# Optimization experiments

Hardware: AMD Instinct MI355X
Metric: run time of the kernel (lower is better)

## Reference

```python
import jax, jax.numpy as jnp
import numpy as np

EPS_NORM = 1e-4
EPS_LOG = 1e-6


def normed_weight(W):
    # W: [O, I, K] (K=1). normalize() over dims (1,2) per output channel,
    # with norm scaled by alpha = sqrt(O / (O*I*K)) = 1/sqrt(I*K), then
    # divided again by sqrt(I*K) in get_normed_weight (eval path).
    O, I, K = W.shape
    fan_in = I * K
    norm = jnp.sqrt(jnp.sum(jnp.square(W), axis=(1, 2), keepdims=True))  # [O,1,1]
    norm = EPS_NORM + norm / np.sqrt(fan_in)
    return (W / norm) / np.sqrt(fan_in)


def complex_log(x):
    real = jnp.log(jnp.maximum(jnp.abs(x), EPS_LOG))
    imag = jnp.where(x < 0, jnp.pi, 0.0).astype(real.dtype)
    return jax.lax.complex(real, imag)


def logcumsumexp_complex(z, axis=-1):
    # stable complex logcumsumexp via associative scan:
    # logaddexp(a, b) = m + log(exp(a-m) + exp(b-m)), m = max(Re a, Re b)
    def combine(a, b):
        m = jnp.maximum(a.real, b.real)
        mc = jax.lax.complex(m, jnp.zeros_like(m))
        return mc + jnp.log(jnp.exp(a - mc) + jnp.exp(b - mc))
    return jax.lax.associative_scan(combine, z, axis=axis)


def min_gru(h, g):
    # h, g: [B, C, L]; parallel log-space minGRU recurrence along L
    log_scale = 0.5 * jnp.log(1.0 / jnp.cosh(g) + 1.0)
    log_coeffs = -jax.nn.softplus(g) + log_scale                 # real
    log_values = (-jax.nn.softplus(-g) + log_scale) + complex_log(h)  # complex
    a_star = jnp.cumsum(log_coeffs, axis=-1)                     # real
    a_star_c = jax.lax.complex(a_star, jnp.zeros_like(a_star))
    log_h = a_star_c + logcumsumexp_complex(log_values - a_star_c, axis=-1)
    return jnp.exp(log_h).real


def scaled_cat(xs, axis):
    Ns = [x.shape[axis] for x in xs]
    scale = np.sqrt(np.mean(Ns))
    return scale * jnp.concatenate([x * n ** -0.5 for n, x in zip(Ns, xs)], axis=axis)


def setup_inputs() -> dict:
    key = jax.random.key(0)
    k1, k2 = jax.random.split(key)
    B, D, L = 8, 512, 8192
    x = jax.random.normal(k1, (B, D, L), dtype=jnp.float32)
    W = jax.random.normal(k2, (2 * D, D, 1), dtype=jnp.float32)  # Conv1d(dim, 2*dim, 1) weight
    return {"x": x, "W": W}


def reference(x, W):
    Wn = normed_weight(W)  # [2D, D, 1]
    fb = jnp.einsum('oi,bil->bol', Wn[:, :, 0], x)  # [B, 2D, L]
    fore, back = jnp.split(fb, 2, axis=1)
    h_f, g_f = jnp.split(fore, 2, axis=1)
    back_r = back[..., ::-1]
    h_b, g_b = jnp.split(back_r, 2, axis=1)
    out_f = min_gru(h_f, g_f)
    out_b = min_gru(h_b, g_b)[..., ::-1]
    return scaled_cat([out_f, out_b], axis=1)
```

## Files before the change

kernel.cpp:

```cpp
#include <hip/hip_runtime.h>
#include <math.h>
#include <stdint.h>

#define LSEQ 8192
#define DIN  512
#define NB   8
#define NO   1024

typedef __bf16 bf16x8 __attribute__((ext_vector_type(8)));
typedef float f32x16 __attribute__((ext_vector_type(16)));

__device__ __forceinline__ uint32_t pack_bf16_rne(float lo, float hi) {
    uint32_t ul = __builtin_bit_cast(uint32_t, lo);
    uint32_t uh = __builtin_bit_cast(uint32_t, hi);
    ul += 0x7FFFu + ((ul >> 16) & 1u);
    uh += 0x7FFFu + ((uh >> 16) & 1u);
    return (ul >> 16) | (uh & 0xFFFF0000u);
}
__device__ __forceinline__ float bf16_lo(uint32_t w) {
    return __builtin_bit_cast(float, w << 16);
}
__device__ __forceinline__ float bf16_hi(uint32_t w) {
    return __builtin_bit_cast(float, w & 0xFFFF0000u);
}

__global__ void norm_kernel(const float* __restrict__ W, uint32_t* __restrict__ Wnb) {
    const int o = blockIdx.x;
    const int lane = threadIdx.x;
    const float* row = W + (size_t)o * DIN;
    float4 v0 = *(const float4*)(row + lane * 4);
    float4 v1 = *(const float4*)(row + 256 + lane * 4);
    float s = v0.x * v0.x + v0.y * v0.y + v0.z * v0.z + v0.w * v0.w
            + v1.x * v1.x + v1.y * v1.y + v1.z * v1.z + v1.w * v1.w;
#pragma unroll
    for (int m = 32; m; m >>= 1) s += __shfl_xor(s, m, 64);
    const float sq = 22.62741699796952f;
    const float scale = 1.0f / ((1e-4f + sqrtf(s) / sq) * sq);
    uint2 w0, w1;
    w0.x = pack_bf16_rne(v0.x * scale, v0.y * scale);
    w0.y = pack_bf16_rne(v0.z * scale, v0.w * scale);
    w1.x = pack_bf16_rne(v1.x * scale, v1.y * scale);
    w1.y = pack_bf16_rne(v1.z * scale, v1.w * scale);
    *(uint2*)&Wnb[o * 256 + lane * 2] = w0;
    *(uint2*)&Wnb[o * 256 + 128 + lane * 2] = w1;
}

__global__ __launch_bounds__(256)
void gemm_kernel(const uint16_t* __restrict__ Wnb, const float* __restrict__ x,
                 uint32_t* __restrict__ fbp) {
    __shared__ uint32_t sA[2048];
    __shared__ uint32_t sB[16 * 132];

    const int tid  = threadIdx.x;
    const int lane = tid & 63;
    const int w    = tid >> 6;
    const int wm   = w & 1, wn = w >> 1;

    const int bx  = blockIdx.x;
    const int xcd = bx & 7;
    const int t   = bx >> 3;
    const int o0  = (t & 7) * 128;
    const int l0  = (xcd + ((t >> 3) << 3)) * 128;
    const int b   = blockIdx.y;

    const float* xb = x + (size_t)b * DIN * LSEQ + l0;

    const int am = tid >> 1;
    const int aq = (tid & 1) * 2;
    const uint16_t* arow = Wnb + (size_t)(o0 + am) * DIN + aq * 8;
    const uint32_t aw0 = am * 16 + ((aq ^ (am & 3)) * 4);
    const uint32_t aw1 = am * 16 + (((aq + 1) ^ (am & 3)) * 4);

    const int k2a = tid >> 5, lqa = tid & 31;
    const int k2b = (tid + 256) >> 5, lqb = tid & 31;

    f32x16 acc[2][2];
#pragma unroll
    for (int i = 0; i < 2; ++i)
#pragma unroll
        for (int j = 0; j < 2; ++j)
#pragma unroll
            for (int r = 0; r < 16; ++r) acc[i][j][r] = 0.f;

    uint4 aR0, aR1;
    float4 bR0, bR1, bR2, bR3;
    {
        aR0 = *(const uint4*)(arow);
        aR1 = *(const uint4*)(arow + 8);
        const float* p0 = xb + (size_t)(2 * k2a) * LSEQ + lqa * 4;
        bR0 = *(const float4*)(p0);
        bR1 = *(const float4*)(p0 + LSEQ);
        const float* p1 = xb + (size_t)(2 * k2b) * LSEQ + lqb * 4;
        bR2 = *(const float4*)(p1);
        bR3 = *(const float4*)(p1 + LSEQ);
    }

#pragma unroll 1
    for (int it = 0; it < 16; ++it) {
        __syncthreads();
        *(uint4*)&sA[aw0] = aR0;
        *(uint4*)&sA[aw1] = aR1;
        {
            uint4 w0, w1;
            w0.x = pack_bf16_rne(bR0.x, bR1.x);
            w0.y = pack_bf16_rne(bR0.y, bR1.y);
            w0.z = pack_bf16_rne(bR0.z, bR1.z);
            w0.w = pack_bf16_rne(bR0.w, bR1.w);
            *(uint4*)&sB[k2a * 132 + lqa * 4] = w0;
            w1.x = pack_bf16_rne(bR2.x, bR3.x);
            w1.y = pack_bf16_rne(bR2.y, bR3.y);
            w1.z = pack_bf16_rne(bR2.z, bR3.z);
            w1.w = pack_bf16_rne(bR2.w, bR3.w);
            *(uint4*)&sB[k2b * 132 + lqb * 4] = w1;
        }
        __syncthreads();
        if (it + 1 < 16) {
            const int kt = (it + 1) * 32;
            aR0 = *(const uint4*)(arow + kt);
            aR1 = *(const uint4*)(arow + kt + 8);
            const float* p0 = xb + (size_t)(kt + 2 * k2a) * LSEQ + lqa * 4;
            bR0 = *(const float4*)(p0);
            bR1 = *(const float4*)(p0 + LSEQ);
            const float* p1 = xb + (size_t)(kt + 2 * k2b) * LSEQ + lqb * 4;
            bR2 = *(const float4*)(p1);
            bR3 = *(const float4*)(p1 + LSEQ);
        }
#pragma unroll
        for (int kh = 0; kh < 2; ++kh) {
            bf16x8 af[2], bfr[2];
#pragma unroll
            for (int ms = 0; ms < 2; ++ms) {
                const int m = wm * 64 + ms * 32 + (lane & 31);
                const int q = kh * 2 + (lane >> 5);
                af[ms] = *(const bf16x8*)&sA[m * 16 + ((q ^ (m & 3)) * 4)];
            }
#pragma unroll
            for (int ns = 0; ns < 2; ++ns) {
                const int col = wn * 64 + ns * 32 + (lane & 31);
                const int rb = kh * 8 + (lane >> 5) * 4;
                uint4 tt;
                tt.x = sB[(rb + 0) * 132 + col];
                tt.y = sB[(rb + 1) * 132 + col];
                tt.z = sB[(rb + 2) * 132 + col];
                tt.w = sB[(rb + 3) * 132 + col];
                bfr[ns] = __builtin_bit_cast(bf16x8, tt);
            }
#pragma unroll
            for (int ms = 0; ms < 2; ++ms)
#pragma unroll
                for (int ns = 0; ns < 2; ++ns)
                    acc[ms][ns] = __builtin_amdgcn_mfma_f32_32x32x16_bf16(
                        af[ms], bfr[ns], acc[ms][ns], 0, 0, 0);
        }
    }

    uint32_t* fbp_b = fbp + (size_t)b * 512 * LSEQ + l0;
#pragma unroll
    for (int ms = 0; ms < 2; ++ms)
#pragma unroll
        for (int ns = 0; ns < 2; ++ns) {
            const f32x16 a = acc[ms][ns];
            const int rb = o0 + wm * 64 + ms * 32 + 4 * (lane >> 5);
            const int cc = wn * 64 + ns * 32 + (lane & 31);
#pragma unroll
            for (int rp = 0; rp < 8; ++rp) {
                const int r = rp * 2;
                const int row = rb + (r & 3) + 8 * (r >> 2);
                fbp_b[(size_t)(row >> 1) * LSEQ + cc] = pack_bf16_rne(a[r], a[r + 1]);
            }
        }
}

__global__ __launch_bounds__(512)
void scan_kernel(const uint32_t* __restrict__ fbp, float* __restrict__ out) {
    __shared__ uint32_t sbuf[8][2048];
    __shared__ float sA0[8], sB0[8], sA1[8], sB1[8];

    const int bx  = blockIdx.x;
    const int b   = blockIdx.y;
    const int dir = bx >> 7;
    const int p   = bx & 127;
    const int o2h = dir * 256 + p;
    const int o2g = dir * 256 + 128 + p;

    const int t    = threadIdx.x;
    const int lane = t & 63;
    const int w    = t >> 6;

    const uint32_t* hwp = fbp + ((size_t)b * 512 + o2h) * LSEQ + w * 1024;
    const uint32_t* gwp = fbp + ((size_t)b * 512 + o2g) * LSEQ + w * 1024;
    uint32_t* sw = sbuf[w];
    float* swf = (float*)sbuf[w];

#pragma unroll
    for (int i = 0; i < 4; ++i) {
        uint4 v = *(const uint4*)(hwp + i * 256 + lane * 4);
        const uint32_t g = i * 64 + lane;
        const uint32_t gs = g ^ ((g >> 3) & 7);
        *(uint4*)&sw[gs * 4] = v;
    }
#pragma unroll
    for (int i = 0; i < 4; ++i) {
        uint4 v = *(const uint4*)(gwp + i * 256 + lane * 4);
        const uint32_t g = i * 64 + lane;
        const uint32_t gs = g ^ ((g >> 3) & 7);
        *(uint4*)&sw[1024 + gs * 4] = v;
    }
    asm volatile("s_waitcnt lgkmcnt(0)" ::: "memory");

    float av0[16], vv0[16], av1[16], vv1[16];
#pragma unroll
    for (int q = 0; q < 4; ++q) {
        const uint32_t g = lane * 4 + q;
        const uint32_t gs = g ^ ((g >> 3) & 7);
        uint4 hw4 = *(const uint4*)&sw[gs * 4];
        uint4 gw4 = *(const uint4*)&sw[1024 + gs * 4];
        const uint32_t hws[4] = {hw4.x, hw4.y, hw4.z, hw4.w};
        const uint32_t gws[4] = {gw4.x, gw4.y, gw4.z, gw4.w};
#pragma unroll
        for (int s = 0; s < 4; ++s) {
            const int mo = q * 4 + s;
            {
                float g_ = fminf(fmaxf(bf16_lo(gws[s]), -30.f), 30.f);
                float eg = __expf(g_);
                float a  = rsqrtf(fmaf(eg, eg, 1.f));
                float h_ = bf16_lo(hws[s]);
                av0[mo] = a;
                vv0[mo] = a * eg * copysignf(fmaxf(fabsf(h_), 1e-6f), h_);
            }
            {
                float g_ = fminf(fmaxf(bf16_hi(gws[s]), -30.f), 30.f);
                float eg = __expf(g_);
                float a  = rsqrtf(fmaf(eg, eg, 1.f));
                float h_ = bf16_hi(hws[s]);
                av1[mo] = a;
                vv1[mo] = a * eg * copysignf(fmaxf(fabsf(h_), 1e-6f), h_);
            }
        }
    }

    float A0 = 1.f, B0 = 0.f, A1 = 1.f, B1 = 0.f;
    if (dir == 0) {
#pragma unroll
        for (int i = 0; i < 16; ++i) {
            B0 = fmaf(av0[i], B0, vv0[i]); A0 *= av0[i];
            B1 = fmaf(av1[i], B1, vv1[i]); A1 *= av1[i];
        }
    } else {
#pragma unroll
        for (int i = 15; i >= 0; --i) {
            B0 = fmaf(av0[i], B0, vv0[i]); A0 *= av0[i];
            B1 = fmaf(av1[i], B1, vv1[i]); A1 *= av1[i];
        }
    }

    if (dir == 0) {
#pragma unroll
        for (int off = 1; off < 64; off <<= 1) {
            float Ap0 = __shfl_up(A0, (unsigned)off, 64), Bp0 = __shfl_up(B0, (unsigned)off, 64);
            float Ap1 = __shfl_up(A1, (unsigned)off, 64), Bp1 = __shfl_up(B1, (unsigned)off, 64);
            if (lane >= off) {
                B0 = fmaf(A0, Bp0, B0); A0 *= Ap0;
                B1 = fmaf(A1, Bp1, B1); A1 *= Ap1;
            }
        }
        if (lane == 63) { sA0[w] = A0; sB0[w] = B0; sA1[w] = A1; sB1[w] = B1; }
    } else {
#pragma unroll
        for (int off = 1; off < 64; off <<= 1) {
            float Ap0 = __shfl_down(A0, (unsigned)off, 64), Bp0 = __shfl_down(B0, (unsigned)off, 64);
            float Ap1 = __shfl_down(A1, (unsigned)off, 64), Bp1 = __shfl_down(B1, (unsigned)off, 64);
            if (lane + off < 64) {
                B0 = fmaf(A0, Bp0, B0); A0 *= Ap0;
                B1 = fmaf(A1, Bp1, B1); A1 *= Ap1;
            }
        }
        if (lane == 0) { sA0[w] = A0; sB0[w] = B0; sA1[w] = A1; sB1[w] = B1; }
    }
    __syncthreads();
    float WB0 = 0.f, WB1 = 0.f;
    if (dir == 0) {
        for (int wv = 0; wv < w; ++wv) {
            WB0 = fmaf(sA0[wv], WB0, sB0[wv]);
            WB1 = fmaf(sA1[wv], WB1, sB1[wv]);
        }
    } else {
        for (int wv = 7; wv > w; --wv) {
            WB0 = fmaf(sA0[wv], WB0, sB0[wv]);
            WB1 = fmaf(sA1[wv], WB1, sB1[wv]);
        }
    }
    float eA0, eB0, eA1, eB1;
    if (dir == 0) {
        eA0 = __shfl_up(A0, 1u, 64); eB0 = __shfl_up(B0, 1u, 64);
        eA1 = __shfl_up(A1, 1u, 64); eB1 = __shfl_up(B1, 1u, 64);
        if (lane == 0) { eA0 = 1.f; eB0 = 0.f; eA1 = 1.f; eB1 = 0.f; }
    } else {
        eA0 = __shfl_down(A0, 1u, 64); eB0 = __shfl_down(B0, 1u, 64);
        eA1 = __shfl_down(A1, 1u, 64); eB1 = __shfl_down(B1, 1u, 64);
        if (lane == 63) { eA0 = 1.f; eB0 = 0.f; eA1 = 1.f; eB1 = 0.f; }
    }
    float H0 = fmaf(eA0, WB0, eB0);
    float H1 = fmaf(eA1, WB1, eB1);

    if (dir == 0) {
#pragma unroll
        for (int i = 0; i < 16; ++i) {
            H0 = fmaf(av0[i], H0, vv0[i]); vv0[i] = H0;
            H1 = fmaf(av1[i], H1, vv1[i]); vv1[i] = H1;
        }
    } else {
#pragma unroll
        for (int i = 15; i >= 0; --i) {
            H0 = fmaf(av0[i], H0, vv0[i]); vv0[i] = H0;
            H1 = fmaf(av1[i], H1, vv1[i]); vv1[i] = H1;
        }
    }

#pragma unroll
    for (int q = 0; q < 4; ++q) {
        const uint32_t g = lane * 4 + q;
        const uint32_t gs = g ^ ((g >> 3) & 7);
        *(float4*)&swf[gs * 4] =
            make_float4(vv0[q * 4], vv0[q * 4 + 1], vv0[q * 4 + 2], vv0[q * 4 + 3]);
        *(float4*)&swf[1024 + gs * 4] =
            make_float4(vv1[q * 4], vv1[q * 4 + 1], vv1[q * 4 + 2], vv1[q * 4 + 3]);
    }
    asm volatile("s_waitcnt lgkmcnt(0)" ::: "memory");
    const int c0 = 2 * p, c1 = 2 * p + 1;
    float* orow0 = out + ((size_t)b * 512 + dir * 256 + c0) * LSEQ + w * 1024;
    float* orow1 = out + ((size_t)b * 512 + dir * 256 + c1) * LSEQ + w * 1024;
#pragma unroll
    for (int i = 0; i < 4; ++i) {
        const uint32_t g = i * 64 + lane;
        const uint32_t gs = g ^ ((g >> 3) & 7);
        *(float4*)(orow0 + i * 256 + lane * 4) = *(const float4*)&swf[gs * 4];
        *(float4*)(orow1 + i * 256 + lane * 4) = *(const float4*)&swf[1024 + gs * 4];
    }
}

extern "C" void kernel_launch(void* const* d_in, const int* in_sizes, int n_in,
                              void* d_out, int out_size, void* d_ws, size_t ws_size,
                              hipStream_t stream) {
    const float* x = (const float*)d_in[0];
    const float* W = (const float*)d_in[1];
    float* out = (float*)d_out;

    uint32_t* Wnb = (uint32_t*)d_ws;
    uint32_t* fbp = (uint32_t*)((char*)d_ws + (size_t)NO * DIN * 2);

    norm_kernel<<<dim3(NO), dim3(64), 0, stream>>>(W, Wnb);
    gemm_kernel<<<dim3(512, NB), dim3(256), 0, stream>>>((const uint16_t*)Wnb, x, fbp);
    scan_kernel<<<dim3(256, NB), dim3(512), 0, stream>>>(fbp, out);
}
```

Baseline: 356.3 us.

## Pre-pack x to bf16 tiles and stream GEMM operands via direct global-to-LDS loads

Adds an xpack kernel that converts x to bf16 and transposes it into K-contiguous tiles per L block. The GEMM then loads A and B straight into double-buffered LDS with global_load_lds, removing the register round trip, the in-loop bf16 packing and one barrier per iteration. The cost is an extra kernel launch and an extra write and read of the packed x (about 64MB written and read back), plus more workspace.

```diff
diff --git a/kernel.cpp b/kernel.cpp
--- a/kernel.cpp
+++ b/kernel.cpp
@@ -22,6 +22,12 @@
 }
 __device__ __forceinline__ float bf16_hi(uint32_t w) {
     return __builtin_bit_cast(float, w & 0xFFFF0000u);
+}
+
+__device__ __forceinline__ void gl_lds16(const void* g, void* l) {
+    __builtin_amdgcn_global_load_lds(
+        (const __attribute__((address_space(1))) void*)g,
+        (__attribute__((address_space(3))) void*)l, 16, 0, 0);
 }
 
 __global__ void norm_kernel(const float* __restrict__ W, uint32_t* __restrict__ Wnb) {
@@ -46,10 +52,51 @@
 }
 
 __global__ __launch_bounds__(256)
-void gemm_kernel(const uint16_t* __restrict__ Wnb, const float* __restrict__ x,
+void xpack_kernel(const float* __restrict__ x, uint32_t* __restrict__ xp) {
+    __shared__ uint32_t sT[32 * 132];
+    const int t  = threadIdx.x;
+    const int bx = blockIdx.x;
+    const int b  = blockIdx.y;
+    const int lt = bx >> 3;
+    const int ch = bx & 7;
+
+    const float* xb = x + (size_t)b * DIN * LSEQ + lt * 128;
+#pragma unroll
+    for (int j = 0; j < 4; ++j) {
+        const int idx = j * 256 + t;
+        const int k2l = idx >> 5;
+        const int lg  = idx & 31;
+        const float* r0 = xb + (size_t)(2 * (ch * 32 + k2l)) * LSEQ + lg * 4;
+        float4 a = *(const float4*)r0;
+        float4 c = *(const float4*)(r0 + LSEQ);
+        uint4 wv;
+        wv.x = pack_bf16_rne(a.x, c.x);
+        wv.y = pack_bf16_rne(a.y, c.y);
+        wv.z = pack_bf16_rne(a.z, c.z);
+        wv.w = pack_bf16_rne(a.w, c.w);
+        *(uint4*)&sT[k2l * 132 + lg * 4] = wv;
+    }
+    __syncthreads();
+    uint32_t* ob = xp + ((size_t)(b * 64 + lt) * 128) * 256 + ch * 32;
+#pragma unroll
+    for (int j = 0; j < 4; ++j) {
+        const int idx = j * 256 + t;
+        const int lp  = idx >> 3;
+        const int gq  = idx & 7;
+        uint4 wv;
+        wv.x = sT[(gq * 4 + 0) * 132 + lp];
+        wv.y = sT[(gq * 4 + 1) * 132 + lp];
+        wv.z = sT[(gq * 4 + 2) * 132 + lp];
+        wv.w = sT[(gq * 4 + 3) * 132 + lp];
+        *(uint4*)&ob[(size_t)lp * 256 + gq * 4] = wv;
+    }
+}
+
+__global__ __launch_bounds__(256)
+void gemm_kernel(const uint32_t* __restrict__ WnbW, const uint32_t* __restrict__ xp,
                  uint32_t* __restrict__ fbp) {
-    __shared__ uint32_t sA[2048];
-    __shared__ uint32_t sB[16 * 132];
+    __shared__ uint32_t sA[2][2048];
+    __shared__ uint32_t sB[2][2048];
 
     const int tid  = threadIdx.x;
     const int lane = tid & 63;
@@ -60,19 +107,17 @@
     const int xcd = bx & 7;
     const int t   = bx >> 3;
     const int o0  = (t & 7) * 128;
-    const int l0  = (xcd + ((t >> 3) << 3)) * 128;
+    const int ltg = xcd + ((t >> 3) << 3);
+    const int l0  = ltg * 128;
     const int b   = blockIdx.y;
 
-    const float* xb = x + (size_t)b * DIN * LSEQ + l0;
-
-    const int am = tid >> 1;
-    const int aq = (tid & 1) * 2;
-    const uint16_t* arow = Wnb + (size_t)(o0 + am) * DIN + aq * 8;
-    const uint32_t aw0 = am * 16 + ((aq ^ (am & 3)) * 4);
-    const uint32_t aw1 = am * 16 + (((aq + 1) ^ (am & 3)) * 4);
-
-    const int k2a = tid >> 5, lqa = tid & 31;
-    const int k2b = (tid + 256) >> 5, lqb = tid & 31;
+    const int rsub = lane >> 2;
+    const int ssub = (lane & 3) ^ (rsub & 3);
+    const uint32_t* gA0 = WnbW + (size_t)(o0 + w * 32 + rsub) * 256 + ssub * 4;
+    const uint32_t* gA1 = gA0 + (size_t)16 * 256;
+    const uint32_t* xptb = xp + (size_t)(b * 64 + ltg) * 32768;
+    const uint32_t* gB0 = xptb + (size_t)(w * 32 + rsub) * 256 + ssub * 4;
+    const uint32_t* gB1 = gB0 + (size_t)16 * 256;
 
     f32x16 acc[2][2];
 #pragma unroll
@@ -82,68 +127,35 @@
 #pragma unroll
             for (int r = 0; r < 16; ++r) acc[i][j][r] = 0.f;
 
-    uint4 aR0, aR1;
-    float4 bR0, bR1, bR2, bR3;
-    {
-        aR0 = *(const uint4*)(arow);
-        aR1 = *(const uint4*)(arow + 8);
-        const float* p0 = xb + (size_t)(2 * k2a) * LSEQ + lqa * 4;
-        bR0 = *(const float4*)(p0);
-        bR1 = *(const float4*)(p0 + LSEQ);
-        const float* p1 = xb + (size_t)(2 * k2b) * LSEQ + lqb * 4;
-        bR2 = *(const float4*)(p1);
-        bR3 = *(const float4*)(p1 + LSEQ);
-    }
-
-#pragma unroll 1
+#define STAGE(it, bs)                                      \
+    do {                                                   \
+        gl_lds16(gA0 + (it) * 16, &sA[bs][w * 512]);       \
+        gl_lds16(gA1 + (it) * 16, &sA[bs][w * 512 + 256]); \
+        gl_lds16(gB0 + (it) * 16, &sB[bs][w * 512]);       \
+        gl_lds16(gB1 + (it) * 16, &sB[bs][w * 512 + 256]); \
+    } while (0)
+
+    STAGE(0, 0);
+#pragma unroll 2
     for (int it = 0; it < 16; ++it) {
+        const int cb = it & 1;
         __syncthreads();
-        *(uint4*)&sA[aw0] = aR0;
-        *(uint4*)&sA[aw1] = aR1;
-        {
-            uint4 w0, w1;
-            w0.x = pack_bf16_rne(bR0.x, bR1.x);
-            w0.y = pack_bf16_rne(bR0.y, bR1.y);
-            w0.z = pack_bf16_rne(bR0.z, bR1.z);
-            w0.w = pack_bf16_rne(bR0.w, bR1.w);
-            *(uint4*)&sB[k2a * 132 + lqa * 4] = w0;
-            w1.x = pack_bf16_rne(bR2.x, bR3.x);
-            w1.y = pack_bf16_rne(bR2.y, bR3.y);
-            w1.z = pack_bf16_rne(bR2.z, bR3.z);
-            w1.w = pack_bf16_rne(bR2.w, bR3.w);
-            *(uint4*)&sB[k2b * 132 + lqb * 4] = w1;
-        }
-        __syncthreads();
-        if (it + 1 < 16) {
-            const int kt = (it + 1) * 32;
-            aR0 = *(const uint4*)(arow + kt);
-            aR1 = *(const uint4*)(arow + kt + 8);
-            const float* p0 = xb + (size_t)(kt + 2 * k2a) * LSEQ + lqa * 4;
-            bR0 = *(const float4*)(p0);
-            bR1 = *(const float4*)(p0 + LSEQ);
-            const float* p1 = xb + (size_t)(kt + 2 * k2b) * LSEQ + lqb * 4;
-            bR2 = *(const float4*)(p1);
-            bR3 = *(const float4*)(p1 + LSEQ);
-        }
+        if (it + 1 < 16) STAGE(it + 1, cb ^ 1);
+        const uint32_t* cA = sA[cb];
+        const uint32_t* cB = sB[cb];
 #pragma unroll
         for (int kh = 0; kh < 2; ++kh) {
+            const int q = kh * 2 + (lane >> 5);
             bf16x8 af[2], bfr[2];
 #pragma unroll
             for (int ms = 0; ms < 2; ++ms) {
                 const int m = wm * 64 + ms * 32 + (lane & 31);
-                const int q = kh * 2 + (lane >> 5);
-                af[ms] = *(const bf16x8*)&sA[m * 16 + ((q ^ (m & 3)) * 4)];
+                af[ms] = *(const bf16x8*)&cA[m * 16 + ((q ^ (m & 3)) << 2)];
             }
 #pragma unroll
             for (int ns = 0; ns < 2; ++ns) {
                 const int col = wn * 64 + ns * 32 + (lane & 31);
-                const int rb = kh * 8 + (lane >> 5) * 4;
-                uint4 tt;
-                tt.x = sB[(rb + 0) * 132 + col];
-                tt.y = sB[(rb + 1) * 132 + col];
-                tt.z = sB[(rb + 2) * 132 + col];
-                tt.w = sB[(rb + 3) * 132 + col];
-                bfr[ns] = __builtin_bit_cast(bf16x8, tt);
+                bfr[ns] = *(const bf16x8*)&cB[col * 16 + ((q ^ (col & 3)) << 2)];
             }
 #pragma unroll
             for (int ms = 0; ms < 2; ++ms)
@@ -153,6 +165,7 @@
                         af[ms], bfr[ns], acc[ms][ns], 0, 0, 0);
         }
     }
+#undef STAGE
 
     uint32_t* fbp_b = fbp + (size_t)b * 512 * LSEQ + l0;
 #pragma unroll
@@ -348,8 +361,11 @@
 
     uint32_t* Wnb = (uint32_t*)d_ws;
     uint32_t* fbp = (uint32_t*)((char*)d_ws + (size_t)NO * DIN * 2);
+    uint32_t* xp  = (uint32_t*)((char*)d_ws + (size_t)NO * DIN * 2
+                                + (size_t)NB * 512 * LSEQ * 4);
 
     norm_kernel<<<dim3(NO), dim3(64), 0, stream>>>(W, Wnb);
-    gemm_kernel<<<dim3(512, NB), dim3(256), 0, stream>>>((const uint16_t*)Wnb, x, fbp);
+    xpack_kernel<<<dim3(512, NB), dim3(256), 0, stream>>>(x, xp);
+    gemm_kernel<<<dim3(512, NB), dim3(256), 0, stream>>>((const uint32_t*)Wnb, xp, fbp);
     scan_kernel<<<dim3(256, NB), dim3(512), 0, stream>>>(fbp, out);
 }
```

After: 365.0 us. 1.02x slower.
